# Performance work log

Measured on AMD Instinct MI355X. Metric: run time of the kernel, lower is better.

## Reference

```python
import jax, jax.numpy as jnp
import numpy as np

EMBED = 1024
HEADS = 16
HEAD_DIM = EMBED // HEADS          # 64
EXP_DIM = 2 * HEAD_DIM             # 128


def setup_inputs() -> dict:
    key = jax.random.key(0)
    ks = jax.random.split(key, 7)
    N, S = 4, 2048
    values = jax.random.normal(ks[0], (N, S, EMBED), dtype=jnp.float32)
    keys_ = jax.random.normal(ks[1], (N, S, EMBED), dtype=jnp.float32)
    query = jax.random.normal(ks[2], (N, S, EMBED), dtype=jnp.float32)
    # feature map linear: initialized to identity weight, zero bias (per init_weights),
    # perturb slightly so it's a nontrivial learned map
    fm_w = jnp.eye(HEAD_DIM, dtype=jnp.float32) + 0.02 * jax.random.normal(ks[3], (HEAD_DIM, HEAD_DIM), dtype=jnp.float32)
    fm_b = 0.02 * jax.random.normal(ks[4], (HEAD_DIM,), dtype=jnp.float32)
    fc_w = jax.random.normal(ks[5], (EMBED, HEADS * EXP_DIM), dtype=jnp.float32) * (1.0 / np.sqrt(HEADS * EXP_DIM))
    fc_b = jnp.zeros((EMBED,), dtype=jnp.float32)
    return {"values": values, "keys": keys_, "query": query,
            "fm_w": fm_w, "fm_b": fm_b, "fc_w": fc_w, "fc_b": fc_b}


def _feature_map(x, fm_w, fm_b):
    # x: [n, s, h, d] -> [n, s, h, 2d]
    z = jnp.einsum('nshd,ed->nshe', x, fm_w) + fm_b
    return jnp.concatenate([jnp.exp(z), jnp.exp(-z)], axis=-1)


def reference(values, keys, query, fm_w, fm_b, fc_w, fc_b):
    N, S, _ = query.shape
    v = values.reshape(N, -1, HEADS, HEAD_DIM)
    k = keys.reshape(N, -1, HEADS, HEAD_DIM)
    q = query.reshape(N, -1, HEADS, HEAD_DIM)
    v, k, q = (_feature_map(x, fm_w, fm_b) for x in (v, k, q))  # [n,s,h,2d]
    scores = jnp.einsum('nqhd,nkhd->nhqk', q, k) / jnp.sqrt(jnp.float32(EMBED))
    attn = jax.nn.softmax(scores, axis=-1)
    out = jnp.einsum('nhql,nlhd->nqhd', attn, v)  # [n,q,h,2d]
    out = out.reshape(N, S, HEADS * EXP_DIM)
    return out @ fc_w.T + fc_b
```

## Files before the change

kernel.cpp:

```cpp
#include <hip/hip_runtime.h>
#include <hip/hip_bf16.h>
#include <stdint.h>

#define N_B 4
#define SEQ 2048
#define NH 16
#define ED 128
#define EMB 1024
#define FCK 2048

typedef float f32x4 __attribute__((ext_vector_type(4)));
typedef float f32x16 __attribute__((ext_vector_type(16)));
typedef _Float16 f16x8 __attribute__((ext_vector_type(8)));
typedef _Float16 f16x4 __attribute__((ext_vector_type(4)));
typedef _Float16 f16x2 __attribute__((ext_vector_type(2)));
typedef __fp16 fp16v2 __attribute__((ext_vector_type(2)));

__device__ __forceinline__ void gload16(const void* g, void* l) {
    __builtin_amdgcn_global_load_lds(
        (const __attribute__((address_space(1))) uint32_t*)(g),
        (__attribute__((address_space(3))) uint32_t*)(l), 16, 0, 0);
}

__device__ __forceinline__ int pk2(float a, float b) {
    union { fp16v2 h; int i; } u;
    u.h = __builtin_amdgcn_cvt_pkrtz(a, b);
    return u.i;
}

__device__ __forceinline__ f16x2 asf16x2(int v) {
    union { int i; f16x2 h; } u; u.i = v; return u.h;
}

__device__ __forceinline__ f16x8 frag4(int d0, int d1, int d2, int d3) {
    union { int i[4]; f16x8 v; } u;
    u.i[0] = d0; u.i[1] = d1; u.i[2] = d2; u.i[3] = d3;
    return u.v;
}

__device__ __forceinline__ float ex2(float x) {
#if __has_builtin(__builtin_amdgcn_exp2f)
    return __builtin_amdgcn_exp2f(x);
#else
    return exp2f(x);
#endif
}

#define LOG2E 1.4426950408889634f
#define M3(a,b,c) fmaxf(fmaxf((a),(b)),(c))

__global__ __launch_bounds__(256) void fmap_kernel(
    const float* __restrict__ vals, const float* __restrict__ keys,
    const float* __restrict__ qry,  const float* __restrict__ fmw,
    const float* __restrict__ fmb,
    _Float16* __restrict__ qf, _Float16* __restrict__ kf,
    _Float16* __restrict__ vf)
{
    const int lane = threadIdx.x & 63;
    const int w = threadIdx.x >> 6;
    const int t = blockIdx.x * 4 + w;
    const int n = t >> 11;
    const int s = t & 2047;
    const int r = lane & 15;
    const int g = lane >> 4;

    f16x8 whf[4][2], wlf[4][2];
    #pragma unroll
    for (int te = 0; te < 4; ++te) {
      #pragma unroll
      for (int j = 0; j < 2; ++j) {
        const float* p = fmw + (te*16 + r)*64 + j*32 + 8*g;
        #pragma unroll
        for (int i = 0; i < 8; ++i) {
            float wv = p[i];
            _Float16 hi = (_Float16)wv;
            whf[te][j][i] = hi;
            wlf[te][j][i] = (_Float16)(wv - (float)hi);
        }
      }
    }
    float bias[4];
    #pragma unroll
    for (int te = 0; te < 4; ++te) bias[te] = fmb[te*16 + r];

    const float QSCL = 0.03125f * LOG2E;

    const long rowoff = ((long)t*16 + r) * 64;
    const float* srcs[3] = {qry, keys, vals};
    #pragma unroll
    for (int tens = 0; tens < 3; ++tens) {
        const float* src = srcs[tens] + rowoff;
        f16x8 ah[2], al[2];
        #pragma unroll
        for (int j = 0; j < 2; ++j) {
            #pragma unroll
            for (int i = 0; i < 8; ++i) {
                float x = src[j*32 + 8*g + i];
                _Float16 hi = (_Float16)x;
                ah[j][i] = hi;
                al[j][i] = (_Float16)(x - (float)hi);
            }
        }
        #pragma unroll
        for (int te = 0; te < 4; ++te) {
            f32x4 c = (f32x4){0.f,0.f,0.f,0.f};
            c = __builtin_amdgcn_mfma_f32_16x16x32_f16(ah[0], whf[te][0], c, 0, 0, 0);
            c = __builtin_amdgcn_mfma_f32_16x16x32_f16(ah[1], whf[te][1], c, 0, 0, 0);
            c = __builtin_amdgcn_mfma_f32_16x16x32_f16(ah[0], wlf[te][0], c, 0, 0, 0);
            c = __builtin_amdgcn_mfma_f32_16x16x32_f16(ah[1], wlf[te][1], c, 0, 0, 0);
            c = __builtin_amdgcn_mfma_f32_16x16x32_f16(al[0], whf[te][0], c, 0, 0, 0);
            c = __builtin_amdgcn_mfma_f32_16x16x32_f16(al[1], whf[te][1], c, 0, 0, 0);
            #pragma unroll
            for (int i = 0; i < 4; ++i) {
                float zl = (c[i] + bias[te]) * LOG2E;
                float ep = ex2(zl), en = ex2(-zl);
                int hh = 4*g + i;
                int e = te*16 + r;
                long base = (((long)n*NH + hh)*SEQ + s)*ED;
                if (tens == 0) {
                    qf[base + e]      = (_Float16)(ep * QSCL);
                    qf[base + 64 + e] = (_Float16)(en * QSCL);
                } else if (tens == 1) {
                    kf[base + e]      = (_Float16)ep;
                    kf[base + 64 + e] = (_Float16)en;
                } else {
                    vf[base + e]      = (_Float16)ep;
                    vf[base + 64 + e] = (_Float16)en;
                }
            }
        }
    }
}

__global__ __launch_bounds__(256) void vtrans_kernel(
    const _Float16* __restrict__ vf, _Float16* __restrict__ vt)
{
    __shared__ _Float16 tile[64][72];
    const int b = blockIdx.x;
    const int et = b & 1;
    const int st = (b >> 1) & 31;
    const int nh = b >> 6;
    const _Float16* src = vf + ((long)nh*SEQ + st*64)*ED + et*64;
    const int col4 = (threadIdx.x & 15) * 4;
    const int row0 = threadIdx.x >> 4;
    #pragma unroll
    for (int j = 0; j < 4; ++j) {
        int row = row0 + j*16;
        *(f16x4*)&tile[row][col4] = *(const f16x4*)(src + (long)row*ED + col4);
    }
    __syncthreads();
    _Float16* dst = vt + ((long)nh*ED + et*64)*SEQ + st*64;
    const int erow = threadIdx.x >> 2;
    const int sc0 = (threadIdx.x & 3) * 16;
    f16x8 o0, o1;
    #pragma unroll
    for (int i = 0; i < 8; ++i) o0[i] = tile[sc0 + i][erow];
    #pragma unroll
    for (int i = 0; i < 8; ++i) o1[i] = tile[sc0 + 8 + i][erow];
    *(f16x8*)(dst + (long)erow*SEQ + sc0) = o0;
    *(f16x8*)(dst + (long)erow*SEQ + sc0 + 8) = o1;
}

__global__ __launch_bounds__(256) void cvt_kernel(
    const float* __restrict__ src, _Float16* __restrict__ dst)
{
    long i = ((long)blockIdx.x*256 + threadIdx.x)*8;
    f16x8 o;
    #pragma unroll
    for (int j = 0; j < 8; ++j) o[j] = (_Float16)src[i + j];
    *(f16x8*)(dst + i) = o;
}

__global__ __launch_bounds__(512, 2) void attn_kernel(
    const _Float16* __restrict__ qf,
    const _Float16* __restrict__ kf,
    const _Float16* __restrict__ vt,
    _Float16* __restrict__ ob)
{
    __shared__ char smem[131072];
    const int tid = threadIdx.x;
    const int lane = tid & 63;
    const int w = tid >> 6;
    const int orig = blockIdx.x;
    const int b = ((orig & 7) << 6) | (orig >> 3);
    const int nh = b >> 3;
    const int n = nh >> 4, h = nh & 15;
    const int qt = (b & 7)*8 + w;
    const int q32 = lane & 31;
    const int hl = lane >> 5;

    const _Float16* qb = qf + (long)nh*SEQ*ED;
    const char* kg = (const char*)(kf + (long)nh*SEQ*ED);
    const char* vg = (const char*)(vt + (long)nh*ED*SEQ);

    f16x8 qfr[8];
    #pragma unroll
    for (int j = 0; j < 8; ++j)
        qfr[j] = *(const f16x8*)(qb + (long)(qt*32 + q32)*ED + 16*j + 8*hl);

    const int srow = tid >> 4;
    const int sc   = (tid & 15) ^ (srow & 15);
    const long koff = (long)srow*256  + sc*16;
    const long voff = (long)srow*4096 + sc*16;
    const int  ldst = tid*16;

    auto stage = [&](int kt, int bsel) {
        char* Kl = smem + bsel*65536;
        char* Vl = Kl + 32768;
        const char* ksrc = kg + (long)kt*32768 + koff;
        const char* vsrc = vg + (long)kt*256   + voff;
        #pragma unroll
        for (int i = 0; i < 4; ++i)
            gload16(ksrc + i*8192, Kl + i*8192 + ldst);
        #pragma unroll
        for (int i = 0; i < 4; ++i)
            gload16(vsrc + (long)i*131072, Vl + i*8192 + ldst);
    };

    f32x16 acc[4];
    #pragma unroll
    for (int vv = 0; vv < 4; ++vv)
      #pragma unroll
      for (int i = 0; i < 16; ++i) acc[vv][i] = 0.f;
    float mrun = 0.f, lrun = 0.f;

    stage(0, 0);
    __syncthreads();

    const int kswz = q32 & 15;

    for (int kt = 0; kt < SEQ/128; ++kt) {
        const int cur = kt & 1;
        if (kt + 1 < SEQ/128) stage(kt + 1, cur ^ 1);
        const char* Kl = smem + cur*65536;
        const char* Vl = Kl + 32768;

        #pragma unroll
        for (int p = 0; p < 2; ++p) {
            const float nmr = -mrun;
            f32x16 s0, s1;
            #pragma unroll
            for (int i = 0; i < 16; ++i) { s0[i] = nmr; s1[i] = nmr; }
            const char* Kb = Kl + (p*64 + q32)*256;
            __builtin_amdgcn_s_setprio(1);
            #pragma unroll
            for (int j = 0; j < 8; ++j) {
                int off = (((hl + 2*j) & 15) ^ kswz) << 4;
                f16x8 k0 = *(const f16x8*)(Kb + off);
                f16x8 k1 = *(const f16x8*)(Kb + 8192 + off);
                s0 = __builtin_amdgcn_mfma_f32_32x32x16_f16(k0, qfr[j], s0, 0, 0, 0);
                s1 = __builtin_amdgcn_mfma_f32_32x32x16_f16(k1, qfr[j], s1, 0, 0, 0);
            }
            __builtin_amdgcn_s_setprio(0);

            float mx = M3(s0[0], s0[1], s0[2]);
            mx = M3(mx, s0[3], s0[4]);   mx = M3(mx, s0[5], s0[6]);
            mx = M3(mx, s0[7], s0[8]);   mx = M3(mx, s0[9], s0[10]);
            mx = M3(mx, s0[11], s0[12]); mx = M3(mx, s0[13], s0[14]);
            mx = M3(mx, s0[15], s1[0]);  mx = M3(mx, s1[1], s1[2]);
            mx = M3(mx, s1[3], s1[4]);   mx = M3(mx, s1[5], s1[6]);
            mx = M3(mx, s1[7], s1[8]);   mx = M3(mx, s1[9], s1[10]);
            mx = M3(mx, s1[11], s1[12]); mx = M3(mx, s1[13], s1[14]);
            mx = fmaxf(mx, s1[15]);
            mx = fmaxf(mx, __shfl_xor(mx, 32, 64));
            if (__any(mx > 8.0f)) {
                float d = fmaxf(mx, 0.f);
                float corr = ex2(-d);
                mrun += d;
                lrun *= corr;
                #pragma unroll
                for (int vv = 0; vv < 4; ++vv)
                    #pragma unroll
                    for (int i = 0; i < 16; ++i) acc[vv][i] *= corr;
                #pragma unroll
                for (int i = 0; i < 16; ++i) { s0[i] -= d; s1[i] -= d; }
            }
            int wreg[2][8];
            f16x2 psum = (f16x2){(_Float16)0.f, (_Float16)0.f};
            #pragma unroll
            for (int tW = 0; tW < 8; ++tW) {
                int pw = pk2(ex2(s0[2*tW]), ex2(s0[2*tW+1]));
                wreg[0][tW] = pw; psum += asf16x2(pw);
            }
            #pragma unroll
            for (int tW = 0; tW < 8; ++tW) {
                int pw = pk2(ex2(s1[2*tW]), ex2(s1[2*tW+1]));
                wreg[1][tW] = pw; psum += asf16x2(pw);
            }
            float rsum = (float)psum[0] + (float)psum[1];
            rsum += __shfl_xor(rsum, 32, 64);
            lrun += rsum;

            f16x8 pa[4];
            #pragma unroll
            for (int kk = 0; kk < 2; ++kk) {
                #pragma unroll
                for (int par = 0; par < 2; ++par) {
                    int a0 = wreg[kk][par*4 + 0], b0 = wreg[kk][par*4 + 2];
                    int a1 = wreg[kk][par*4 + 1], b1 = wreg[kk][par*4 + 3];
                    auto r0 = __builtin_amdgcn_permlane32_swap(a0, b0, false, false);
                    auto r1 = __builtin_amdgcn_permlane32_swap(a1, b1, false, false);
                    pa[kk*2 + par] = frag4(r0[0], r1[0], r0[1], r1[1]);
                }
            }

            #pragma unroll
            for (int ks = 0; ks < 4; ++ks) {
                f16x8 vfr[4];
                #pragma unroll
                for (int vv = 0; vv < 4; ++vv) {
                    int vrow = vv*32 + q32;
                    int c0 = p*8 + ks*2 + hl;
                    vfr[vv] = *(const f16x8*)(Vl + vrow*256 + ((c0 ^ kswz) << 4));
                }
                __builtin_amdgcn_s_setprio(1);
                #pragma unroll
                for (int vv = 0; vv < 4; ++vv)
                    acc[vv] = __builtin_amdgcn_mfma_f32_32x32x16_f16(vfr[vv], pa[ks], acc[vv], 0, 0, 0);
                __builtin_amdgcn_s_setprio(0);
            }
        }
        __syncthreads();
    }

    float inv = 1.0f / lrun;
    int q = qt*32 + q32;
    long base = ((long)n*SEQ + q)*FCK + h*ED;
    #pragma unroll
    for (int vv = 0; vv < 4; ++vv) {
        #pragma unroll
        for (int rg = 0; rg < 4; ++rg) {
            f16x4 o;
            #pragma unroll
            for (int i = 0; i < 4; ++i) o[i] = (_Float16)(acc[vv][rg*4 + i] * inv);
            *(f16x4*)(ob + base + vv*32 + 8*rg + 4*hl) = o;
        }
    }
}

__global__ __launch_bounds__(256) void fc_kernel(
    const _Float16* __restrict__ ob,
    const _Float16* __restrict__ wt,
    const float* __restrict__ fcb,
    float* __restrict__ out)
{
    __shared__ char smem[65536];
    const int tid = threadIdx.x;
    const int lane = tid & 63;
    const int w = tid >> 6;
    const int wm = w >> 1, wn = w & 1;
    const int r = lane & 15, g = lane >> 4;

    const int orig = blockIdx.x;
    const int tile = ((orig & 7) << 6) | (orig >> 3);
    const int mt = tile >> 3;
    const int nt = tile & 7;

    const char* Ag = (const char*)(ob + (long)mt*128*FCK);
    const char* Bg = (const char*)(wt + (long)nt*128*FCK);

    const int srow = tid >> 3;
    const int schk = tid & 7;
    const int  ldst = tid*16;
    const long goff = (long)srow*(FCK*2) + (schk ^ (srow & 7))*16;

    auto stage = [&](int kt, int bsel) {
        char* As = smem + bsel*32768;
        char* Bs = As + 16384;
        const char* asrc = Ag + (long)kt*128 + goff;
        const char* bsrc = Bg + (long)kt*128 + goff;
        #pragma unroll
        for (int rnd = 0; rnd < 4; ++rnd)
            gload16(asrc + (long)rnd*32*(FCK*2), As + rnd*4096 + ldst);
        #pragma unroll
        for (int rnd = 0; rnd < 4; ++rnd)
            gload16(bsrc + (long)rnd*32*(FCK*2), Bs + rnd*4096 + ldst);
    };

    f32x4 acc[4][4];
    #pragma unroll
    for (int u = 0; u < 4; ++u)
      #pragma unroll
      for (int v = 0; v < 4; ++v) acc[u][v] = (f32x4){0.f,0.f,0.f,0.f};

    stage(0, 0);
    __syncthreads();

    for (int kt = 0; kt < FCK/64; ++kt) {
        const int cur = kt & 1;
        if (kt + 1 < FCK/64) stage(kt + 1, cur ^ 1);
        const char* As = smem + cur*32768;
        const char* Bs = As + 16384;

        #pragma unroll
        for (int kk = 0; kk < 2; ++kk) {
            f16x8 afr[4], bfr[4];
            #pragma unroll
            for (int u = 0; u < 4; ++u) {
                int row = wm*64 + u*16 + r;
                afr[u] = *(const f16x8*)(As + row*128 + (((g + 4*kk) ^ (row & 7)) << 4));
            }
            #pragma unroll
            for (int v = 0; v < 4; ++v) {
                int row = wn*64 + v*16 + r;
                bfr[v] = *(const f16x8*)(Bs + row*128 + (((g + 4*kk) ^ (row & 7)) << 4));
            }
            __builtin_amdgcn_s_setprio(1);
            #pragma unroll
            for (int u = 0; u < 4; ++u)
              #pragma unroll
              for (int v = 0; v < 4; ++v)
                acc[u][v] = __builtin_amdgcn_mfma_f32_16x16x32_f16(afr[u], bfr[v], acc[u][v], 0, 0, 0);
            __builtin_amdgcn_s_setprio(0);
        }
        __syncthreads();
    }

    #pragma unroll
    for (int u = 0; u < 4; ++u)
      #pragma unroll
      for (int v = 0; v < 4; ++v) {
        int col = nt*128 + wn*64 + v*16 + r;
        float bias = fcb[col];
        #pragma unroll
        for (int i = 0; i < 4; ++i) {
            int row = mt*128 + wm*64 + u*16 + 4*g + i;
            out[(long)row*EMB + col] = acc[u][v][i] + bias;
        }
      }
}

extern "C" void kernel_launch(void* const* d_in, const int* in_sizes, int n_in,
                              void* d_out, int out_size, void* d_ws, size_t ws_size,
                              hipStream_t stream) {
    const float* vals = (const float*)d_in[0];
    const float* keys = (const float*)d_in[1];
    const float* qry  = (const float*)d_in[2];
    const float* fmw  = (const float*)d_in[3];
    const float* fmb  = (const float*)d_in[4];
    const float* fcw  = (const float*)d_in[5];
    const float* fcb  = (const float*)d_in[6];
    char* ws = (char*)d_ws;
    const long SZ = 33554432L;
    _Float16* qf = (_Float16*)(ws);
    _Float16* kf = (_Float16*)(ws + SZ);
    _Float16* vf = (_Float16*)(ws + 2*SZ);
    _Float16* vt = (_Float16*)(ws + 3*SZ);
    _Float16* ob = (_Float16*)(ws + 4*SZ);
    _Float16* wt = (_Float16*)(ws + 5*SZ);
    float* out = (float*)d_out;

    fmap_kernel<<<dim3(2048), dim3(256), 0, stream>>>(vals, keys, qry, fmw, fmb, qf, kf, vf);
    vtrans_kernel<<<dim3(4096), dim3(256), 0, stream>>>(vf, vt);
    cvt_kernel<<<dim3(1024), dim3(256), 0, stream>>>(fcw, wt);
    attn_kernel<<<dim3(512), dim3(512), 0, stream>>>(qf, kf, vt, ob);
    fc_kernel<<<dim3(512), dim3(256), 0, stream>>>(ob, wt, fcb, out);
}
```

Before: 266.3 us.

## Fuse V transpose into feature-map kernel via shared-memory tile

The separate vtrans kernel is removed. The feature-map kernel now assigns each block 64 sequence rows of one head and stages the V feature outputs in a shared tile, then writes them transposed directly to vt. This removes a launch and a full round trip of the V intermediate through global memory. The block-to-data mapping also changes, which alters the input read pattern (each wave now reads 16 rows of one head at a 1024-float stride) and adds a __syncthreads plus LDS traffic.

```diff
diff --git a/kernel.cpp b/kernel.cpp
--- a/kernel.cpp
+++ b/kernel.cpp
@@ -54,13 +54,16 @@
     const float* __restrict__ qry,  const float* __restrict__ fmw,
     const float* __restrict__ fmb,
     _Float16* __restrict__ qf, _Float16* __restrict__ kf,
-    _Float16* __restrict__ vf)
+    _Float16* __restrict__ vt)
 {
-    const int lane = threadIdx.x & 63;
-    const int w = threadIdx.x >> 6;
-    const int t = blockIdx.x * 4 + w;
-    const int n = t >> 11;
-    const int s = t & 2047;
+    __shared__ _Float16 vtile[64][136];
+    const int tid = threadIdx.x;
+    const int lane = tid & 63;
+    const int w = tid >> 6;
+    const int b = blockIdx.x;
+    const int st = b & 31;
+    const int h  = (b >> 5) & 15;
+    const int n  = b >> 9;
     const int r = lane & 15;
     const int g = lane >> 4;
 
@@ -85,7 +88,8 @@
 
     const float QSCL = 0.03125f * LOG2E;
 
-    const long rowoff = ((long)t*16 + r) * 64;
+    const int s0 = st*64 + w*16;
+    const long rowoff = ((long)n*SEQ + s0 + r)*EMB + h*64;
     const float* srcs[3] = {qry, keys, vals};
     #pragma unroll
     for (int tens = 0; tens < 3; ++tens) {
@@ -114,51 +118,36 @@
             for (int i = 0; i < 4; ++i) {
                 float zl = (c[i] + bias[te]) * LOG2E;
                 float ep = ex2(zl), en = ex2(-zl);
-                int hh = 4*g + i;
                 int e = te*16 + r;
-                long base = (((long)n*NH + hh)*SEQ + s)*ED;
-                if (tens == 0) {
-                    qf[base + e]      = (_Float16)(ep * QSCL);
-                    qf[base + 64 + e] = (_Float16)(en * QSCL);
-                } else if (tens == 1) {
-                    kf[base + e]      = (_Float16)ep;
-                    kf[base + 64 + e] = (_Float16)en;
+                int srow = 4*g + i;
+                if (tens == 2) {
+                    vtile[w*16 + srow][e]      = (_Float16)ep;
+                    vtile[w*16 + srow][64 + e] = (_Float16)en;
                 } else {
-                    vf[base + e]      = (_Float16)ep;
-                    vf[base + 64 + e] = (_Float16)en;
+                    long base = (((long)(n*NH + h))*SEQ + s0 + srow)*ED;
+                    if (tens == 0) {
+                        qf[base + e]      = (_Float16)(ep * QSCL);
+                        qf[base + 64 + e] = (_Float16)(en * QSCL);
+                    } else {
+                        kf[base + e]      = (_Float16)ep;
+                        kf[base + 64 + e] = (_Float16)en;
+                    }
                 }
             }
         }
     }
-}
-
-__global__ __launch_bounds__(256) void vtrans_kernel(
-    const _Float16* __restrict__ vf, _Float16* __restrict__ vt)
-{
-    __shared__ _Float16 tile[64][72];
-    const int b = blockIdx.x;
-    const int et = b & 1;
-    const int st = (b >> 1) & 31;
-    const int nh = b >> 6;
-    const _Float16* src = vf + ((long)nh*SEQ + st*64)*ED + et*64;
-    const int col4 = (threadIdx.x & 15) * 4;
-    const int row0 = threadIdx.x >> 4;
-    #pragma unroll
-    for (int j = 0; j < 4; ++j) {
-        int row = row0 + j*16;
-        *(f16x4*)&tile[row][col4] = *(const f16x4*)(src + (long)row*ED + col4);
-    }
+
     __syncthreads();
-    _Float16* dst = vt + ((long)nh*ED + et*64)*SEQ + st*64;
-    const int erow = threadIdx.x >> 2;
-    const int sc0 = (threadIdx.x & 3) * 16;
-    f16x8 o0, o1;
-    #pragma unroll
-    for (int i = 0; i < 8; ++i) o0[i] = tile[sc0 + i][erow];
-    #pragma unroll
-    for (int i = 0; i < 8; ++i) o1[i] = tile[sc0 + 8 + i][erow];
-    *(f16x8*)(dst + (long)erow*SEQ + sc0) = o0;
-    *(f16x8*)(dst + (long)erow*SEQ + sc0 + 8) = o1;
+    const int e  = tid >> 1;
+    const int sh = tid & 1;
+    _Float16* dst = vt + ((long)(n*NH + h)*ED + e)*SEQ + st*64 + sh*32;
+    #pragma unroll
+    for (int cchunk = 0; cchunk < 4; ++cchunk) {
+        f16x8 o;
+        #pragma unroll
+        for (int j = 0; j < 8; ++j) o[j] = vtile[sh*32 + cchunk*8 + j][e];
+        *(f16x8*)(dst + cchunk*8) = o;
+    }
 }
 
 __global__ __launch_bounds__(256) void cvt_kernel(
@@ -444,14 +433,12 @@
     const long SZ = 33554432L;
     _Float16* qf = (_Float16*)(ws);
     _Float16* kf = (_Float16*)(ws + SZ);
-    _Float16* vf = (_Float16*)(ws + 2*SZ);
-    _Float16* vt = (_Float16*)(ws + 3*SZ);
-    _Float16* ob = (_Float16*)(ws + 4*SZ);
-    _Float16* wt = (_Float16*)(ws + 5*SZ);
+    _Float16* vt = (_Float16*)(ws + 2*SZ);
+    _Float16* ob = (_Float16*)(ws + 3*SZ);
+    _Float16* wt = (_Float16*)(ws + 4*SZ);
     float* out = (float*)d_out;
 
-    fmap_kernel<<<dim3(2048), dim3(256), 0, stream>>>(vals, keys, qry, fmw, fmb, qf, kf, vf);
-    vtrans_kernel<<<dim3(4096), dim3(256), 0, stream>>>(vf, vt);
+    fmap_kernel<<<dim3(2048), dim3(256), 0, stream>>>(vals, keys, qry, fmw, fmb, qf, kf, vt);
     cvt_kernel<<<dim3(1024), dim3(256), 0, stream>>>(fcw, wt);
     attn_kernel<<<dim3(512), dim3(512), 0, stream>>>(qf, kf, vt, ob);
     fc_kernel<<<dim3(512), dim3(256), 0, stream>>>(ob, wt, fcb, out);
```

After: 246.9 us. -7.3%, faster.
